# Kernel tuning notes

Hardware: AMD Instinct MI355X
Metric: run time of the kernel (lower is better)

Reference implementation:

```python
import jax, jax.numpy as jnp
import numpy as np

TOP_K = 2


def setup_inputs() -> dict:
    key = jax.random.key(0)
    k1, k2 = jax.random.split(key)
    x = jax.random.normal(k1, (4, 4096, 2048), dtype=jnp.float32)
    W = jax.random.normal(k2, (64, 2048), dtype=jnp.float32) * (1.0 / np.sqrt(2048))
    return {"x": x, "W": W}


def reference(x, W):
    B, S, D = x.shape
    E = W.shape[0]
    # logits: [B*S, E] via linear router (no bias)
    flat = x.reshape(-1, D)
    logits = jnp.einsum('td,ed->te', flat, W)
    probs = jax.nn.softmax(logits, axis=-1)
    # eval path: top-k indices
    _, top_k_indices = jax.lax.top_k(probs, TOP_K)          # [T, K]
    # scatter 1s -> mask; scatter gathered probs -> router_probs (== probs*mask)
    router_mask = jax.nn.one_hot(top_k_indices, E, dtype=probs.dtype).sum(axis=-2)  # [T, E]
    router_probs = probs * router_mask
    # normalize (top_k > 1: gradient flows through the sum)
    router_probs = router_probs / router_probs.sum(axis=-1, keepdims=True)
    return (router_mask.reshape(B, S, E),
            top_k_indices.reshape(B, S, TOP_K),
            router_probs.reshape(B, S, E),
            probs.reshape(B, S, E))
```

## Files before the change

### kernel.cpp

```cpp
#include <hip/hip_runtime.h>
#include <math.h>


#define D_DIM 2048
#define E_DIM 64

typedef __bf16 bf16x8 __attribute__((ext_vector_type(8)));
typedef unsigned short us8 __attribute__((ext_vector_type(8)));
typedef float f32x4 __attribute__((ext_vector_type(4)));

static __device__ __forceinline__ unsigned short f2bf(float f) {
    unsigned int u = __float_as_uint(f);
    u += 0x7fffu + ((u >> 16) & 1u);
    return (unsigned short)(u >> 16);
}
static __device__ __forceinline__ float bf2f(unsigned short h) {
    return __uint_as_float(((unsigned int)h) << 16);
}
static __device__ __forceinline__ void split4(const float4 v, ushort4* h, ushort4* l) {
    h->x = f2bf(v.x); l->x = f2bf(v.x - bf2f(h->x));
    h->y = f2bf(v.y); l->y = f2bf(v.y - bf2f(h->y));
    h->z = f2bf(v.z); l->z = f2bf(v.z - bf2f(h->z));
    h->w = f2bf(v.w); l->w = f2bf(v.w - bf2f(h->w));
}

static __device__ __forceinline__ void gld_lds16(const void* g, void* l) {
    __builtin_amdgcn_global_load_lds(
        (const __attribute__((address_space(1))) unsigned int*)g,
        (__attribute__((address_space(3))) unsigned int*)l,
        16, 0, 0);
}

__global__ __launch_bounds__(256, 1) void convert_w(
    const float4* __restrict__ W4, unsigned short* __restrict__ WH,
    unsigned short* __restrict__ WL)
{
    int i = blockIdx.x * 256 + threadIdx.x;
    float4 v = W4[i];
    ushort4 h, l;
    split4(v, &h, &l);
    *(ushort4*)&WH[i * 4] = h;
    *(ushort4*)&WL[i * 4] = l;
}

template<int KS>
__global__ __launch_bounds__(256, 4) void gemm_part(
    const float* __restrict__ x,
    const unsigned short* __restrict__ WHg, const unsigned short* __restrict__ WLg,
    float* __restrict__ P, int T)
{
    __shared__ __align__(16) float          XF [64 * 64];
    __shared__ __align__(16) unsigned short WHs[64 * 64];
    __shared__ __align__(16) unsigned short WLs[64 * 64];

    const int tid  = threadIdx.x;
    const int lane = tid & 63;
    const int wv   = tid >> 6;
    const int quad = lane >> 4;
    const int l16  = lane & 15;

    const int ntb = T >> 6;
    const int tb  = blockIdx.x % ntb;
    const int ksl = blockIdx.x / ntb;
    const int t0  = tb << 6;
    const int NCH = (D_DIM / KS) >> 6;
    const int k0  = ksl * (D_DIM / KS);

    f32x4 acc[4];
    #pragma unroll
    for (int n = 0; n < 4; ++n) { f32x4 z = {0.f, 0.f, 0.f, 0.f}; acc[n] = z; }

    const int srow = wv * 4 + (lane >> 4);
    const int scg  = lane & 15;
    const int we   = wv * 8 + (lane >> 3);
    const int wo   = lane & 7;

    for (int ch = 0; ch < NCH; ++ch) {
        const int kc = k0 + (ch << 6);

        #pragma unroll
        for (int i = 0; i < 4; ++i) {
            int row = i * 16 + srow;
            int cg  = scg ^ (row & 15);
            gld_lds16(x + (size_t)(t0 + row) * D_DIM + kc + cg * 4,
                      &XF[(i * 256 + wv * 64) * 4]);
        }
        #pragma unroll
        for (int i2 = 0; i2 < 2; ++i2) {
            int e  = i2 * 32 + we;
            int og = wo ^ (e & 7);
            gld_lds16(WHg + (size_t)e * D_DIM + kc + og * 8,
                      &WHs[(i2 * 256 + wv * 64) * 8]);
            gld_lds16(WLg + (size_t)e * D_DIM + kc + og * 8,
                      &WLs[(i2 * 256 + wv * 64) * 8]);
        }
        __syncthreads();

        #pragma unroll
        for (int ks = 0; ks < 2; ++ks) {
            const int tr = wv * 16 + l16;
            const int c0 = ks * 8 + quad * 2;
            float4 xa = *(const float4*)&XF[(tr * 16 + ( c0      ^ (tr & 15))) * 4];
            float4 xb = *(const float4*)&XF[(tr * 16 + ((c0 + 1) ^ (tr & 15))) * 4];
            ushort4 h0, l0, h1, l1;
            split4(xa, &h0, &l0);
            split4(xb, &h1, &l1);
            union { us8 u; bf16x8 b; } ua, ul;
            ua.u = (us8){h0.x, h0.y, h0.z, h0.w, h1.x, h1.y, h1.z, h1.w};
            ul.u = (us8){l0.x, l0.y, l0.z, l0.w, l1.x, l1.y, l1.z, l1.w};

            #pragma unroll
            for (int n = 0; n < 4; ++n) {
                int e = n * 16 + l16;
                int o = ks * 4 + quad;
                int s = e * 8 + (o ^ (e & 7));
                bf16x8 bh = *(const bf16x8*)&WHs[s * 8];
                bf16x8 bl = *(const bf16x8*)&WLs[s * 8];
                acc[n] = __builtin_amdgcn_mfma_f32_16x16x32_bf16(ua.b, bh, acc[n], 0, 0, 0);
                acc[n] = __builtin_amdgcn_mfma_f32_16x16x32_bf16(ul.b, bh, acc[n], 0, 0, 0);
                acc[n] = __builtin_amdgcn_mfma_f32_16x16x32_bf16(ua.b, bl, acc[n], 0, 0, 0);
            }
        }
        __syncthreads();
    }

    float* Pb = P + ((size_t)ksl * T + t0) * 64;
    #pragma unroll
    for (int n = 0; n < 4; ++n)
        #pragma unroll
        for (int r = 0; r < 4; ++r)
            Pb[(wv * 16 + quad * 4 + r) * 64 + n * 16 + l16] = acc[n][r];
}

template<int KS>
__global__ __launch_bounds__(256, 4) void reduce_router(
    const float* __restrict__ P, int T,
    float* __restrict__ mask_out, float* __restrict__ idx_out,
    float* __restrict__ rp_out, float* __restrict__ probs_out)
{
    const int tid  = threadIdx.x;
    const int lane = tid & 63;
    const int wv   = tid >> 6;

    for (int i = 0; i < 4; ++i) {
        int t = blockIdx.x * 16 + wv * 4 + i;
        float v = 0.f;
        #pragma unroll
        for (int s = 0; s < KS; ++s)
            v += P[((size_t)s * T + t) * 64 + lane];

        float bv = v; int bi = lane;
        #pragma unroll
        for (int off = 1; off < 64; off <<= 1) {
            float ov = __shfl_xor(bv, off, 64);
            int   oi = __shfl_xor(bi, off, 64);
            bool take = (ov > bv) || (ov == bv && oi < bi);
            bv = take ? ov : bv;
            bi = take ? oi : bi;
        }
        float m = bv; int i1 = bi;

        float p = __expf(v - m);
        float s = p;
        #pragma unroll
        for (int off = 1; off < 64; off <<= 1) s += __shfl_xor(s, off, 64);
        float prob = p / s;

        float v2 = (lane == i1) ? -INFINITY : v;
        float bv2 = v2; int bi2 = lane;
        #pragma unroll
        for (int off = 1; off < 64; off <<= 1) {
            float ov = __shfl_xor(bv2, off, 64);
            int   oi = __shfl_xor(bi2, off, 64);
            bool take = (ov > bv2) || (ov == bv2 && oi < bi2);
            bv2 = take ? ov : bv2;
            bi2 = take ? oi : bi2;
        }
        int i2 = bi2;

        float pd = __shfl(prob, i1, 64) + __shfl(prob, i2, 64);
        bool top = (lane == i1) || (lane == i2);

        mask_out[(size_t)t * 64 + lane]  = top ? 1.f : 0.f;
        rp_out[(size_t)t * 64 + lane]    = top ? prob / pd : 0.f;
        probs_out[(size_t)t * 64 + lane] = prob;
        if (lane == 0) {
            idx_out[(size_t)t * 2]     = (float)i1;
            idx_out[(size_t)t * 2 + 1] = (float)i2;
        }
    }
}

extern "C" void kernel_launch(void* const* d_in, const int* in_sizes, int n_in,
                              void* d_out, int out_size, void* d_ws, size_t ws_size,
                              hipStream_t stream) {
    const float* x = (const float*)d_in[0];
    const float* W = (const float*)d_in[1];
    float* out = (float*)d_out;

    const int T  = in_sizes[0] / D_DIM;
    const int WN = in_sizes[1];

    unsigned short* WH = (unsigned short*)d_ws;
    unsigned short* WL = WH + WN;
    float* P = (float*)(WL + WN);

    float* mask_out  = out;
    float* idx_out   = out + (size_t)T * E_DIM;
    float* rp_out    = idx_out + (size_t)T * 2;
    float* probs_out = rp_out + (size_t)T * E_DIM;

    const size_t avail = ws_size - (size_t)WN * 4;
    const size_t slice_bytes = (size_t)T * 64 * 4;

    convert_w<<<dim3(WN / 1024), dim3(256), 0, stream>>>((const float4*)W, WH, WL);

    if (avail >= 4 * slice_bytes) {
        gemm_part<4><<<dim3((T / 64) * 4), dim3(256), 0, stream>>>(x, WH, WL, P, T);
        reduce_router<4><<<dim3(T / 16), dim3(256), 0, stream>>>(
            P, T, mask_out, idx_out, rp_out, probs_out);
    } else if (avail >= 2 * slice_bytes) {
        gemm_part<2><<<dim3((T / 64) * 2), dim3(256), 0, stream>>>(x, WH, WL, P, T);
        reduce_router<2><<<dim3(T / 16), dim3(256), 0, stream>>>(
            P, T, mask_out, idx_out, rp_out, probs_out);
    } else {
        gemm_part<1><<<dim3(T / 64), dim3(256), 0, stream>>>(x, WH, WL, P, T);
        reduce_router<1><<<dim3(T / 16), dim3(256), 0, stream>>>(
            P, T, mask_out, idx_out, rp_out, probs_out);
    }
}
```

Before: 209.6 us.

## Fuse router GEMM with softmax/top-k epilogue and double-buffer LDS loads

Drops the split-K partial buffer and separate reduction kernel. The GEMM now runs the full K range per 64-token block and computes softmax, top-2 and the outputs directly from the MFMA accumulators using 16-lane shuffles. It also double-buffers the LDS staging so the next chunk's global loads overlap the current chunk's MFMAs. This removes the partial-sum round trip through global memory and one launch, but grid parallelism falls to T/64 blocks (256 on this shape) with launch_bounds of one block per SM, which may hurt latency hiding.

```diff
diff --git a/kernel.cpp b/kernel.cpp
--- a/kernel.cpp
+++ b/kernel.cpp
@@ -43,15 +43,15 @@
     *(ushort4*)&WL[i * 4] = l;
 }
 
-template<int KS>
-__global__ __launch_bounds__(256, 4) void gemm_part(
+__global__ __launch_bounds__(256, 1) void router_fused(
     const float* __restrict__ x,
     const unsigned short* __restrict__ WHg, const unsigned short* __restrict__ WLg,
-    float* __restrict__ P, int T)
+    float* __restrict__ mask_out, float* __restrict__ idx_out,
+    float* __restrict__ rp_out, float* __restrict__ probs_out)
 {
-    __shared__ __align__(16) float          XF [64 * 64];
-    __shared__ __align__(16) unsigned short WHs[64 * 64];
-    __shared__ __align__(16) unsigned short WLs[64 * 64];
+    __shared__ __align__(16) float          XF [2][64 * 64];
+    __shared__ __align__(16) unsigned short WHs[2][64 * 64];
+    __shared__ __align__(16) unsigned short WLs[2][64 * 64];
 
     const int tid  = threadIdx.x;
     const int lane = tid & 63;
@@ -59,12 +59,8 @@
     const int quad = lane >> 4;
     const int l16  = lane & 15;
 
-    const int ntb = T >> 6;
-    const int tb  = blockIdx.x % ntb;
-    const int ksl = blockIdx.x / ntb;
-    const int t0  = tb << 6;
-    const int NCH = (D_DIM / KS) >> 6;
-    const int k0  = ksl * (D_DIM / KS);
+    const int t0  = blockIdx.x << 6;
+    const int NCH = D_DIM >> 6;
 
     f32x4 acc[4];
     #pragma unroll
@@ -75,33 +71,55 @@
     const int we   = wv * 8 + (lane >> 3);
     const int wo   = lane & 7;
 
-    for (int ch = 0; ch < NCH; ++ch) {
-        const int kc = k0 + (ch << 6);
-
+    {
         #pragma unroll
         for (int i = 0; i < 4; ++i) {
             int row = i * 16 + srow;
             int cg  = scg ^ (row & 15);
-            gld_lds16(x + (size_t)(t0 + row) * D_DIM + kc + cg * 4,
-                      &XF[(i * 256 + wv * 64) * 4]);
+            gld_lds16(x + (size_t)(t0 + row) * D_DIM + cg * 4,
+                      &XF[0][(i * 256 + wv * 64) * 4]);
         }
         #pragma unroll
         for (int i2 = 0; i2 < 2; ++i2) {
             int e  = i2 * 32 + we;
             int og = wo ^ (e & 7);
-            gld_lds16(WHg + (size_t)e * D_DIM + kc + og * 8,
-                      &WHs[(i2 * 256 + wv * 64) * 8]);
-            gld_lds16(WLg + (size_t)e * D_DIM + kc + og * 8,
-                      &WLs[(i2 * 256 + wv * 64) * 8]);
-        }
-        __syncthreads();
+            gld_lds16(WHg + (size_t)e * D_DIM + og * 8,
+                      &WHs[0][(i2 * 256 + wv * 64) * 8]);
+            gld_lds16(WLg + (size_t)e * D_DIM + og * 8,
+                      &WLs[0][(i2 * 256 + wv * 64) * 8]);
+        }
+    }
+    __syncthreads();
+
+    int buf = 0;
+    for (int ch = 0; ch < NCH; ++ch) {
+        if (ch + 1 < NCH) {
+            const int kc = (ch + 1) << 6;
+            const int nb = buf ^ 1;
+            #pragma unroll
+            for (int i = 0; i < 4; ++i) {
+                int row = i * 16 + srow;
+                int cg  = scg ^ (row & 15);
+                gld_lds16(x + (size_t)(t0 + row) * D_DIM + kc + cg * 4,
+                          &XF[nb][(i * 256 + wv * 64) * 4]);
+            }
+            #pragma unroll
+            for (int i2 = 0; i2 < 2; ++i2) {
+                int e  = i2 * 32 + we;
+                int og = wo ^ (e & 7);
+                gld_lds16(WHg + (size_t)e * D_DIM + kc + og * 8,
+                          &WHs[nb][(i2 * 256 + wv * 64) * 8]);
+                gld_lds16(WLg + (size_t)e * D_DIM + kc + og * 8,
+                          &WLs[nb][(i2 * 256 + wv * 64) * 8]);
+            }
+        }
 
         #pragma unroll
         for (int ks = 0; ks < 2; ++ks) {
             const int tr = wv * 16 + l16;
             const int c0 = ks * 8 + quad * 2;
-            float4 xa = *(const float4*)&XF[(tr * 16 + ( c0      ^ (tr & 15))) * 4];
-            float4 xb = *(const float4*)&XF[(tr * 16 + ((c0 + 1) ^ (tr & 15))) * 4];
+            float4 xa = *(const float4*)&XF[buf][(tr * 16 + ( c0      ^ (tr & 15))) * 4];
+            float4 xb = *(const float4*)&XF[buf][(tr * 16 + ((c0 + 1) ^ (tr & 15))) * 4];
             ushort4 h0, l0, h1, l1;
             split4(xa, &h0, &l0);
             split4(xb, &h1, &l1);
@@ -114,77 +132,88 @@
                 int e = n * 16 + l16;
                 int o = ks * 4 + quad;
                 int s = e * 8 + (o ^ (e & 7));
-                bf16x8 bh = *(const bf16x8*)&WHs[s * 8];
-                bf16x8 bl = *(const bf16x8*)&WLs[s * 8];
+                bf16x8 bh = *(const bf16x8*)&WHs[buf][s * 8];
+                bf16x8 bl = *(const bf16x8*)&WLs[buf][s * 8];
                 acc[n] = __builtin_amdgcn_mfma_f32_16x16x32_bf16(ua.b, bh, acc[n], 0, 0, 0);
                 acc[n] = __builtin_amdgcn_mfma_f32_16x16x32_bf16(ul.b, bh, acc[n], 0, 0, 0);
                 acc[n] = __builtin_amdgcn_mfma_f32_16x16x32_bf16(ua.b, bl, acc[n], 0, 0, 0);
             }
         }
         __syncthreads();
+        buf ^= 1;
     }
 
-    float* Pb = P + ((size_t)ksl * T + t0) * 64;
     #pragma unroll
-    for (int n = 0; n < 4; ++n)
-        #pragma unroll
-        for (int r = 0; r < 4; ++r)
-            Pb[(wv * 16 + quad * 4 + r) * 64 + n * 16 + l16] = acc[n][r];
-}
-
-template<int KS>
-__global__ __launch_bounds__(256, 4) void reduce_router(
-    const float* __restrict__ P, int T,
-    float* __restrict__ mask_out, float* __restrict__ idx_out,
-    float* __restrict__ rp_out, float* __restrict__ probs_out)
-{
-    const int tid  = threadIdx.x;
-    const int lane = tid & 63;
-    const int wv   = tid >> 6;
-
-    for (int i = 0; i < 4; ++i) {
-        int t = blockIdx.x * 16 + wv * 4 + i;
-        float v = 0.f;
-        #pragma unroll
-        for (int s = 0; s < KS; ++s)
-            v += P[((size_t)s * T + t) * 64 + lane];
-
-        float bv = v; int bi = lane;
-        #pragma unroll
-        for (int off = 1; off < 64; off <<= 1) {
-            float ov = __shfl_xor(bv, off, 64);
-            int   oi = __shfl_xor(bi, off, 64);
+    for (int r = 0; r < 4; ++r) {
+        const int t = t0 + wv * 16 + quad * 4 + r;
+        const float v0 = acc[0][r], v1 = acc[1][r], v2 = acc[2][r], v3 = acc[3][r];
+
+        float bv = v0; int bi = l16;
+        if (v1 > bv) { bv = v1; bi = 16 + l16; }
+        if (v2 > bv) { bv = v2; bi = 32 + l16; }
+        if (v3 > bv) { bv = v3; bi = 48 + l16; }
+        #pragma unroll
+        for (int off = 1; off < 16; off <<= 1) {
+            float ov = __shfl_xor(bv, off);
+            int   oi = __shfl_xor(bi, off);
             bool take = (ov > bv) || (ov == bv && oi < bi);
             bv = take ? ov : bv;
             bi = take ? oi : bi;
         }
-        float m = bv; int i1 = bi;
-
-        float p = __expf(v - m);
-        float s = p;
-        #pragma unroll
-        for (int off = 1; off < 64; off <<= 1) s += __shfl_xor(s, off, 64);
-        float prob = p / s;
-
-        float v2 = (lane == i1) ? -INFINITY : v;
-        float bv2 = v2; int bi2 = lane;
-        #pragma unroll
-        for (int off = 1; off < 64; off <<= 1) {
-            float ov = __shfl_xor(bv2, off, 64);
-            int   oi = __shfl_xor(bi2, off, 64);
-            bool take = (ov > bv2) || (ov == bv2 && oi < bi2);
-            bv2 = take ? ov : bv2;
-            bi2 = take ? oi : bi2;
-        }
-        int i2 = bi2;
-
-        float pd = __shfl(prob, i1, 64) + __shfl(prob, i2, 64);
-        bool top = (lane == i1) || (lane == i2);
-
-        mask_out[(size_t)t * 64 + lane]  = top ? 1.f : 0.f;
-        rp_out[(size_t)t * 64 + lane]    = top ? prob / pd : 0.f;
-        probs_out[(size_t)t * 64 + lane] = prob;
-        if (lane == 0) {
+        const float m = bv; const int i1 = bi;
+
+        const float p0 = __expf(v0 - m), p1 = __expf(v1 - m);
+        const float p2 = __expf(v2 - m), p3 = __expf(v3 - m);
+        float s = p0 + p1 + p2 + p3;
+        #pragma unroll
+        for (int off = 1; off < 16; off <<= 1) s += __shfl_xor(s, off);
+
+        const float w0 = (i1 == l16)      ? -INFINITY : v0;
+        const float w1 = (i1 == 16 + l16) ? -INFINITY : v1;
+        const float w2 = (i1 == 32 + l16) ? -INFINITY : v2;
+        const float w3 = (i1 == 48 + l16) ? -INFINITY : v3;
+        float cv = w0; int ci = l16;
+        if (w1 > cv) { cv = w1; ci = 16 + l16; }
+        if (w2 > cv) { cv = w2; ci = 32 + l16; }
+        if (w3 > cv) { cv = w3; ci = 48 + l16; }
+        #pragma unroll
+        for (int off = 1; off < 16; off <<= 1) {
+            float ov = __shfl_xor(cv, off);
+            int   oi = __shfl_xor(ci, off);
+            bool take = (ov > cv) || (ov == cv && oi < ci);
+            cv = take ? ov : cv;
+            ci = take ? oi : ci;
+        }
+        const int i2 = ci;
+
+        const float inv_s = 1.f / s;
+        const float q0 = p0 * inv_s, q1 = p1 * inv_s;
+        const float q2 = p2 * inv_s, q3 = p3 * inv_s;
+        const bool m0 = (l16 == i1)      || (l16 == i2);
+        const bool m1 = (16 + l16 == i1) || (16 + l16 == i2);
+        const bool m2 = (32 + l16 == i1) || (32 + l16 == i2);
+        const bool m3 = (48 + l16 == i1) || (48 + l16 == i2);
+
+        float pd = (m0 ? q0 : 0.f) + (m1 ? q1 : 0.f)
+                 + (m2 ? q2 : 0.f) + (m3 ? q3 : 0.f);
+        #pragma unroll
+        for (int off = 1; off < 16; off <<= 1) pd += __shfl_xor(pd, off);
+        const float ipd = 1.f / pd;
+
+        const size_t base = (size_t)t * 64 + l16;
+        probs_out[base]      = q0;
+        probs_out[base + 16] = q1;
+        probs_out[base + 32] = q2;
+        probs_out[base + 48] = q3;
+        mask_out[base]      = m0 ? 1.f : 0.f;
+        mask_out[base + 16] = m1 ? 1.f : 0.f;
+        mask_out[base + 32] = m2 ? 1.f : 0.f;
+        mask_out[base + 48] = m3 ? 1.f : 0.f;
+        rp_out[base]      = m0 ? q0 * ipd : 0.f;
+        rp_out[base + 16] = m1 ? q1 * ipd : 0.f;
+        rp_out[base + 32] = m2 ? q2 * ipd : 0.f;
+        rp_out[base + 48] = m3 ? q3 * ipd : 0.f;
+        if (l16 == 0) {
             idx_out[(size_t)t * 2]     = (float)i1;
             idx_out[(size_t)t * 2 + 1] = (float)i2;
         }
@@ -203,29 +232,13 @@
 
     unsigned short* WH = (unsigned short*)d_ws;
     unsigned short* WL = WH + WN;
-    float* P = (float*)(WL + WN);
 
     float* mask_out  = out;
     float* idx_out   = out + (size_t)T * E_DIM;
     float* rp_out    = idx_out + (size_t)T * 2;
     float* probs_out = rp_out + (size_t)T * E_DIM;
 
-    const size_t avail = ws_size - (size_t)WN * 4;
-    const size_t slice_bytes = (size_t)T * 64 * 4;
-
     convert_w<<<dim3(WN / 1024), dim3(256), 0, stream>>>((const float4*)W, WH, WL);
-
-    if (avail >= 4 * slice_bytes) {
-        gemm_part<4><<<dim3((T / 64) * 4), dim3(256), 0, stream>>>(x, WH, WL, P, T);
-        reduce_router<4><<<dim3(T / 16), dim3(256), 0, stream>>>(
-            P, T, mask_out, idx_out, rp_out, probs_out);
-    } else if (avail >= 2 * slice_bytes) {
-        gemm_part<2><<<dim3((T / 64) * 2), dim3(256), 0, stream>>>(x, WH, WL, P, T);
-        reduce_router<2><<<dim3(T / 16), dim3(256), 0, stream>>>(
-            P, T, mask_out, idx_out, rp_out, probs_out);
-    } else {
-        gemm_part<1><<<dim3(T / 64), dim3(256), 0, stream>>>(x, WH, WL, P, T);
-        reduce_router<1><<<dim3(T / 16), dim3(256), 0, stream>>>(
-            P, T, mask_out, idx_out, rp_out, probs_out);
-    }
-}
+    router_fused<<<dim3(T / 64), dim3(256), 0, stream>>>(
+        x, WH, WL, mask_out, idx_out, rp_out, probs_out);
+}
```

Measured after the change: 225.9 us. 1.08x slower.
